# Optimization experiments

Measured on AMD Instinct MI355X. Metric: run time of the kernel, lower is better.

## Reference

```python
import jax, jax.numpy as jnp
import numpy as np

PI = 3.1415927410125732
N = 4096
VELOCITY = 5e-7
RC = 3.15e-6          # collision radius
RR = 8e-6             # repulsion radius
RO = 2.5e-5           # orientation radius (Ra = inf -> inside_Ra all-true)
ALPHA = PI            # field of view; < 2*pi so within_view masking is active
DT_TRANS = 1.4e-14    # translational diffusion DT
DR = 0.0028
GAMMA = 25.0
DT = 0.2              # timestep dt
COLLISION_ITERS = 3   # fixed-iteration version of recursive solve_collisions
EPS = 1e-14


def _c(x):  # [N,2] real -> complex64
    return jax.lax.complex(x[..., 0], x[..., 1])


def _r(z):  # complex -> [..., 2] real
    return jnp.stack([z.real, z.imag], axis=-1)


def _anglediff(a, b):
    # torch get_anglediff: wrap angle(a)-angle(b) into (-pi, pi)
    diff = jnp.angle(a) - jnp.angle(b)
    diff = jnp.where(diff <= -PI, jnp.mod(diff, PI), diff)
    return diff - (diff >= PI) * (2.0 * PI)


def _cossim(a, b):
    # nn.CosineSimilarity(dim=1, eps=1e-14) on view_as_real of complex vectors
    dot = a.real * b.real + a.imag * b.imag
    na = jnp.sqrt(a.real ** 2 + a.imag ** 2 + 1e-30)
    nb = jnp.sqrt(b.real ** 2 + b.imag ** 2 + 1e-30)
    return dot / (jnp.maximum(na, EPS) * jnp.maximum(nb, EPS))


def setup_inputs() -> dict:
    key = jax.random.key(0)
    k1, k2, k3, k4, k5 = jax.random.split(key, 5)
    positions = jax.random.normal(k1, (N, 2), jnp.float32) * 5e-4
    ang = jax.random.uniform(k2, (N,), jnp.float32, -PI, PI)
    orientations = jnp.stack([jnp.cos(ang), jnp.sin(ang)], axis=-1)  # unit complex
    Deltas = jax.random.uniform(k3, (1,), jnp.float32, 0.1, 0.6)
    rot_noise = jax.random.normal(k4, (N,), jnp.float32)
    trans_noise = jax.random.normal(k5, (N, 2), jnp.float32)
    return {"positions": positions, "orientations": orientations, "Deltas": Deltas,
            "rot_noise": rot_noise, "trans_noise": trans_noise}


def reference(positions, orientations, Deltas, rot_noise, trans_noise):
    p = _c(positions)      # [N] complex positions
    u = _c(orientations)   # [N] complex orientations
    n = p.shape[0]
    eye = jnp.eye(n, dtype=bool)

    # pairwise direction/distance: dirs[i,j] = p_j - p_i
    dirs = p[None, :] - p[:, None]
    dists = jnp.abs(dirs)

    inside_Rr = (dists <= RR) & ~eye
    inside_Ro = dists <= RO + RC
    # inside_Ra with Ra = inf is all-True

    # angle between separation vector and orientation of the *neighbor* j
    ang_diff = _anglediff(dirs, u[None, :])
    in_front = ang_diff < PI / 2
    within_view = ang_diff < ALPHA  # alpha < 2*pi branch active

    cdtype = p.dtype
    mask_rr = (inside_Rr & in_front).astype(cdtype)
    mask_ra = within_view.astype(cdtype)  # inside_Ra all True
    mask_ro = (inside_Ro & within_view).astype(cdtype)

    n_r = mask_rr.real.sum(axis=1)
    S = (mask_rr @ p) / jnp.maximum(n_r, 1.0) - p * jnp.sign(n_r)
    d = -S

    n_a = mask_ra.real.sum(axis=1)
    cms = (mask_ra @ p) / jnp.maximum(n_a, 1.0)
    Ps = cms - p * jnp.sign(n_a)

    orientation_sums = mask_ro @ u

    leftturns = Ps * jnp.exp(1j * Deltas)
    rightturns = Ps * jnp.exp(-1j * Deltas)

    # T >= T_release branch: pick the turn most aligned with neighbor orientations
    left_closer = _cossim(leftturns, orientation_sums) >= _cossim(rightturns, orientation_sums)
    best_turns = jnp.where(left_closer, leftturns, rightturns)

    d_abs = jnp.abs(d)
    d_safe = jnp.where(d_abs > 0, d, jnp.ones((), cdtype))
    best_safe = jnp.where(jnp.abs(best_turns) > 0, best_turns, jnp.ones((), cdtype))
    angle_to_target = jnp.where(d_abs > 0, _anglediff(d_safe, u), _anglediff(best_safe, u))

    # rotational_noise = randn * sqrt(2*DR); rotation = exp(i*(dt*Gamma*DR*sin + noise*sqrt(dt)))
    rot = jnp.exp(1j * (DT * GAMMA * DR * jnp.sin(angle_to_target)
                        + rot_noise * np.float32(np.sqrt(2 * DR)) * np.float32(np.sqrt(DT))))

    # complex-normal translational noise (per-component std 1/sqrt(2)) * sqrt(2*DT) * sqrt(dt)
    tn = _c(trans_noise) * np.float32(np.sqrt(0.5)) * np.float32(np.sqrt(2 * DT_TRANS))
    translation = DT * VELOCITY * u + tn * np.float32(np.sqrt(DT))

    def collide(i, pos):
        dd = pos[None, :] - pos[:, None]
        dd_nd = jnp.where(eye, jnp.ones((), pos.dtype), dd)  # avoid 0/0 on diagonal
        ab = jnp.where(eye, 0.0, jnp.abs(dd_nd))
        coll = ab <= 2 * RC - jnp.eye(n, dtype=ab.dtype)
        safe = jnp.where(coll, ab, 1.0)
        move = jnp.where(coll, dd / safe * ((2.1 * RC - ab) * 0.5), jnp.zeros((), pos.dtype))
        return pos - move.sum(axis=1)

    new_p = jax.lax.fori_loop(0, COLLISION_ITERS, collide, p + translation)
    new_u = u * rot

    # pack the 5 complex outputs as real [5, N, 2]
    return jnp.stack([_r(new_p), _r(new_u), _r(orientation_sums), _r(leftturns), _r(rightturns)], axis=0)
```

## Files before the change

### kernel.cpp

```cpp
#include <hip/hip_runtime.h>
#include <math.h>

#define NPART 4096
#define NBLK  512
#define NTHR  256
#define IPB   8
#define SMAX  512

constexpr float RORC   = (float)(2.5e-5 + 3.15e-6);
constexpr float RORC2  = RORC * RORC;
constexpr float RRF    = 8e-6f;
constexpr float RR2    = RRF * RRF;
constexpr float TWORC  = (float)(2.0 * 3.15e-6);
constexpr float TWORC2 = TWORC * TWORC;
constexpr float C21RC  = (float)(2.1 * 3.15e-6);
constexpr float RCAND2 = 1.6e-9f;
constexpr float C_ROT  = (float)(0.2 * 25.0 * 0.0028);
constexpr float C_RN1  = (float)0.07483314773547883;
constexpr float C_SQDT = (float)0.4472135954999579;
constexpr float C_TRV  = (float)(0.2 * 5e-7);
constexpr float C_HALF = (float)0.7071067811865476;
constexpr float C_SQ2T = (float)1.6733200530681511e-07;
constexpr float EPSF   = 1e-14f;

__global__ __launch_bounds__(NTHR) void fused_all(
        const float2* __restrict__ pos, const float2* __restrict__ ori,
        const float* __restrict__ Deltas, const float* __restrict__ rot_noise,
        const float2* __restrict__ trans_noise, float2* __restrict__ out) {
    __shared__ float4   pp4[NPART / 2];
    __shared__ float2   pori_s[NPART];
    __shared__ float    sred[5 * NTHR];
    __shared__ float    res[5][IPB];
    __shared__ unsigned bmap[NPART / 32];
    __shared__ int      Sidx[SMAX];
    __shared__ float2   posS[SMAX];
    __shared__ int      scnt;
    __shared__ int      iloc[IPB];
    float2* ppos_s = (float2*)pp4;

    const int tid  = threadIdx.x;
    if (tid == 0) scnt = 0;
    if (tid < NPART / 32) bmap[tid] = 0u;
    const int il   = tid & (IPB - 1);
    const int seg  = tid / IPB;
    const int gi   = blockIdx.x * IPB + il;
    const int base = seg * 128;

    for (int k = 0; k < NPART / NTHR; ++k) {
        const int j = k * NTHR + tid;
        ppos_s[j] = pos[j];
        pori_s[j] = ori[j];
    }
    __syncthreads();

    const float2 pi = ppos_s[gi];
    float nr = 0.f, sx = 0.f, sy = 0.f, oxs = 0.f, oys = 0.f;
    #pragma unroll 4
    for (int t = 0; t < 64; ++t) {
        const int k2 = (t + seg) & 63;
        const int j0 = base + 2 * k2;
        const float4 v = pp4[j0 >> 1];
        const float dx0 = v.x - pi.x, dy0 = v.y - pi.y;
        const float dx1 = v.z - pi.x, dy1 = v.w - pi.y;
        const float r20 = fmaf(dx0, dx0, dy0 * dy0);
        const float r21 = fmaf(dx1, dx1, dy1 * dy1);
        if (r20 <= RCAND2) {
            const float2 uj = pori_s[j0];
            if (r20 <= RORC2) { oxs += uj.x; oys += uj.y; }
            if (r20 > 0.f) {
                if (r20 <= RR2) {
                    const float dt_ = fmaf(dx0, uj.x, dy0 * uj.y);
                    const float cr_ = fmaf(dy0, uj.x, -dx0 * uj.y);
                    if (!((dt_ <= 0.f) && (cr_ >= 0.f))) { nr += 1.f; sx += v.x; sy += v.y; }
                }
                atomicOr(&bmap[j0 >> 5], 1u << (j0 & 31));
            }
        }
        if (r21 <= RCAND2) {
            const int j1 = j0 + 1;
            const float2 uj = pori_s[j1];
            if (r21 <= RORC2) { oxs += uj.x; oys += uj.y; }
            if (r21 > 0.f) {
                if (r21 <= RR2) {
                    const float dt_ = fmaf(dx1, uj.x, dy1 * uj.y);
                    const float cr_ = fmaf(dy1, uj.x, -dx1 * uj.y);
                    if (!((dt_ <= 0.f) && (cr_ >= 0.f))) { nr += 1.f; sx += v.z; sy += v.w; }
                }
                atomicOr(&bmap[j1 >> 5], 1u << (j1 & 31));
            }
        }
    }
    if (tid < IPB)
        atomicOr(&bmap[gi >> 5], 1u << (gi & 31));
    __syncthreads();
    sred[0 * NTHR + tid] = nr;
    sred[1 * NTHR + tid] = sx;
    sred[2 * NTHR + tid] = sy;
    sred[3 * NTHR + tid] = oxs;
    sred[4 * NTHR + tid] = oys;
    __syncthreads();
    if (tid < 5 * IPB) {
        const int q = tid / IPB, ii = tid & (IPB - 1);
        float acc = 0.f;
        #pragma unroll
        for (int s = 0; s < 32; ++s) acc += sred[q * NTHR + ii + IPB * s];
        res[q][ii] = acc;
    }
    if (tid >= 64 && tid < 64 + NPART / 32) {
        const int w = tid - 64;
        unsigned bits = bmap[w];
        while (bits) {
            const int b = __ffs(bits) - 1;
            bits &= bits - 1;
            const int p = w * 32 + b;
            const int slot = atomicAdd(&scnt, 1);
            if (slot < SMAX) {
                Sidx[slot] = p;
                if ((p >> 3) == (int)blockIdx.x) iloc[p & (IPB - 1)] = slot;
            }
        }
    }
    __syncthreads();
    const int nS = (scnt < SMAX) ? scnt : SMAX;

    float mx = 0.f, my = 0.f;
    for (int k = 0; k < NPART / NTHR; ++k) {
        const float2 v = ppos_s[k * NTHR + tid];
        mx += v.x; my += v.y;
    }
    sred[tid] = mx; sred[NTHR + tid] = my;
    __syncthreads();
    for (int s = NTHR / 2; s > 0; s >>= 1) {
        if (tid < s) { sred[tid] += sred[tid + s]; sred[NTHR + tid] += sred[NTHR + tid + s]; }
        __syncthreads();
    }
    const float cmx = sred[0]    * (1.f / NPART);
    const float cmy = sred[NTHR] * (1.f / NPART);

    for (int m = tid; m < nS; m += NTHR) {
        const int p = Sidx[m];
        const float2 pp = ppos_s[p];
        const float2 uu = pori_s[p];
        const float2 tn = trans_noise[p];
        posS[m] = make_float2(
            pp.x + (C_TRV * uu.x + ((tn.x * C_HALF) * C_SQ2T) * C_SQDT),
            pp.y + (C_TRV * uu.y + ((tn.y * C_HALF) * C_SQ2T) * C_SQDT));
    }

    if (tid < IPB) {
        const int g2 = blockIdx.x * IPB + tid;
        const float2 p = ppos_s[g2];
        const float2 u = pori_s[g2];
        const float nrv = res[0][tid], sxv = res[1][tid], syv = res[2][tid];
        const float osx = res[3][tid], osy = res[4][tid];

        const float inv = 1.f / fmaxf(nrv, 1.f);
        const float sg  = (nrv > 0.f) ? 1.f : 0.f;
        const float Sx = sxv * inv - p.x * sg;
        const float Sy = syv * inv - p.y * sg;
        const float dxv = -Sx, dyv = -Sy;

        const float Psx = cmx - p.x;
        const float Psy = cmy - p.y;

        float sd, cd;
        sincosf(Deltas[0], &sd, &cd);
        const float Lx = Psx * cd - Psy * sd;
        const float Ly = Psx * sd + Psy * cd;
        const float Rx = Psx * cd + Psy * sd;
        const float Ry = Psy * cd - Psx * sd;

        const float no  = fmaxf(sqrtf(osx * osx + osy * osy + 1e-30f), EPSF);
        const float nl  = fmaxf(sqrtf(Lx * Lx + Ly * Ly + 1e-30f), EPSF);
        const float nrr = fmaxf(sqrtf(Rx * Rx + Ry * Ry + 1e-30f), EPSF);
        const float csl = (Lx * osx + Ly * osy) / (nl * no);
        const float csr = (Rx * osx + Ry * osy) / (nrr * no);
        const bool left = (csl >= csr);
        const float bx = left ? Lx : Rx;
        const float by = left ? Ly : Ry;

        float cx, cy;
        if (dxv != 0.f || dyv != 0.f)    { cx = dxv; cy = dyv; }
        else if (bx != 0.f || by != 0.f) { cx = bx;  cy = by;  }
        else                             { cx = 1.f; cy = 0.f; }

        const float dt_ = cx * u.x + cy * u.y;
        const float cr_ = cy * u.x - cx * u.y;
        const float sin_t = cr_ / sqrtf(dt_ * dt_ + cr_ * cr_);

        const float ang = C_ROT * sin_t + (rot_noise[g2] * C_RN1) * C_SQDT;
        float sa, ca;
        sincosf(ang, &sa, &ca);
        const float nux = u.x * ca - u.y * sa;
        const float nuy = u.x * sa + u.y * ca;

        out[1 * NPART + g2] = make_float2(nux, nuy);
        out[2 * NPART + g2] = make_float2(osx, osy);
        out[3 * NPART + g2] = make_float2(Lx, Ly);
        out[4 * NPART + g2] = make_float2(Rx, Ry);
    }
    __syncthreads();

    for (int pass = 0; pass < 3; ++pass) {
        float ax[2] = {0.f, 0.f}, ay[2] = {0.f, 0.f};
        float px[2], py[2];
        #pragma unroll
        for (int q = 0; q < 2; ++q) {
            const int m = tid + q * NTHR;
            if (m < nS) { px[q] = posS[m].x; py[q] = posS[m].y; }
        }
        for (int b = 0; b < nS; ++b) {
            const float2 pb = posS[b];
            #pragma unroll
            for (int q = 0; q < 2; ++q) {
                const int m = tid + q * NTHR;
                if (m < nS) {
                    const float dx = pb.x - px[q], dy = pb.y - py[q];
                    const float r2 = fmaf(dx, dx, dy * dy);
                    if (r2 <= TWORC2 && r2 > 0.f) {
                        const float ab = sqrtf(r2);
                        const float s = (C21RC - ab) * 0.5f / ab;
                        ax[q] = fmaf(dx, s, ax[q]);
                        ay[q] = fmaf(dy, s, ay[q]);
                    }
                }
            }
        }
        __syncthreads();
        #pragma unroll
        for (int q = 0; q < 2; ++q) {
            const int m = tid + q * NTHR;
            if (m < nS) posS[m] = make_float2(px[q] - ax[q], py[q] - ay[q]);
        }
        __syncthreads();
    }
    if (tid < IPB)
        out[0 * NPART + blockIdx.x * IPB + tid] = posS[iloc[tid]];
}

extern "C" void kernel_launch(void* const* d_in, const int* in_sizes, int n_in,
                              void* d_out, int out_size, void* d_ws, size_t ws_size,
                              hipStream_t stream) {
    const float2* pos = (const float2*)d_in[0];
    const float2* ori = (const float2*)d_in[1];
    const float*  del = (const float*)d_in[2];
    const float*  rn  = (const float*)d_in[3];
    const float2* tn  = (const float2*)d_in[4];
    float2* o2 = (float2*)d_out;
    (void)d_ws; (void)ws_size;

    fused_all<<<dim3(NBLK), dim3(NTHR), 0, stream>>>(pos, ori, del, rn, tn, o2);
}
```

Before: 102.0 us.

## Compact candidate neighbor pairs into list, process via atomics; drop orientation smem staging

The all-pairs scan now only tests distances and appends candidate (i,j) pairs to a shared list instead of evaluating the orientation and repulsion logic inline. A second phase walks that compact list, fetches orientations from global memory on demand, and accumulates the per-particle sums with shared atomics. This removes the orientation staging into LDS and the partial-sum reduction across 256 threads. The collision loop is also unrolled four at a time using float4 loads. The risks are atomic contention and silently truncated results if the pair list exceeds its 1024-entry capacity.

```diff
diff --git a/kernel.cpp b/kernel.cpp
--- a/kernel.cpp
+++ b/kernel.cpp
@@ -5,6 +5,7 @@
 #define NBLK  512
 #define NTHR  256
 #define IPB   8
+#define CAPL  1024
 #define SMAX  512
 
 constexpr float RORC   = (float)(2.5e-5 + 3.15e-6);
@@ -28,86 +29,88 @@
         const float* __restrict__ Deltas, const float* __restrict__ rot_noise,
         const float2* __restrict__ trans_noise, float2* __restrict__ out) {
     __shared__ float4   pp4[NPART / 2];
-    __shared__ float2   pori_s[NPART];
-    __shared__ float    sred[5 * NTHR];
+    __shared__ float    sred[2 * NTHR];
     __shared__ float    res[5][IPB];
     __shared__ unsigned bmap[NPART / 32];
+    __shared__ int      lpairs[CAPL];
     __shared__ int      Sidx[SMAX];
-    __shared__ float2   posS[SMAX];
-    __shared__ int      scnt;
+    __shared__ float4   posS4[SMAX / 2];
+    __shared__ int      lcnt, scnt;
     __shared__ int      iloc[IPB];
     float2* ppos_s = (float2*)pp4;
-
-    const int tid  = threadIdx.x;
-    if (tid == 0) scnt = 0;
+    float2* posS   = (float2*)posS4;
+
+    const int tid = threadIdx.x;
+    if (tid == 0) { lcnt = 0; scnt = 0; }
+    if (tid < 5 * IPB) ((float*)res)[tid] = 0.f;
     if (tid < NPART / 32) bmap[tid] = 0u;
-    const int il   = tid & (IPB - 1);
-    const int seg  = tid / IPB;
-    const int gi   = blockIdx.x * IPB + il;
-    const int base = seg * 128;
-
-    for (int k = 0; k < NPART / NTHR; ++k) {
-        const int j = k * NTHR + tid;
-        ppos_s[j] = pos[j];
-        pori_s[j] = ori[j];
-    }
+    const int il  = tid & (IPB - 1);
+    const int seg = tid / IPB;
+    const int gi  = blockIdx.x * IPB + il;
+
+    for (int k = 0; k < NPART / NTHR; ++k)
+        ppos_s[k * NTHR + tid] = pos[k * NTHR + tid];
     __syncthreads();
 
     const float2 pi = ppos_s[gi];
-    float nr = 0.f, sx = 0.f, sy = 0.f, oxs = 0.f, oys = 0.f;
-    #pragma unroll 4
-    for (int t = 0; t < 64; ++t) {
-        const int k2 = (t + seg) & 63;
-        const int j0 = base + 2 * k2;
-        const float4 v = pp4[j0 >> 1];
-        const float dx0 = v.x - pi.x, dy0 = v.y - pi.y;
-        const float dx1 = v.z - pi.x, dy1 = v.w - pi.y;
-        const float r20 = fmaf(dx0, dx0, dy0 * dy0);
-        const float r21 = fmaf(dx1, dx1, dy1 * dy1);
-        if (r20 <= RCAND2) {
-            const float2 uj = pori_s[j0];
-            if (r20 <= RORC2) { oxs += uj.x; oys += uj.y; }
-            if (r20 > 0.f) {
-                if (r20 <= RR2) {
-                    const float dt_ = fmaf(dx0, uj.x, dy0 * uj.y);
-                    const float cr_ = fmaf(dy0, uj.x, -dx0 * uj.y);
-                    if (!((dt_ <= 0.f) && (cr_ >= 0.f))) { nr += 1.f; sx += v.x; sy += v.y; }
-                }
-                atomicOr(&bmap[j0 >> 5], 1u << (j0 & 31));
-            }
-        }
-        if (r21 <= RCAND2) {
-            const int j1 = j0 + 1;
-            const float2 uj = pori_s[j1];
-            if (r21 <= RORC2) { oxs += uj.x; oys += uj.y; }
-            if (r21 > 0.f) {
-                if (r21 <= RR2) {
-                    const float dt_ = fmaf(dx1, uj.x, dy1 * uj.y);
-                    const float cr_ = fmaf(dy1, uj.x, -dx1 * uj.y);
-                    if (!((dt_ <= 0.f) && (cr_ >= 0.f))) { nr += 1.f; sx += v.z; sy += v.w; }
-                }
-                atomicOr(&bmap[j1 >> 5], 1u << (j1 & 31));
-            }
-        }
-    }
-    if (tid < IPB)
-        atomicOr(&bmap[gi >> 5], 1u << (gi & 31));
-    __syncthreads();
-    sred[0 * NTHR + tid] = nr;
-    sred[1 * NTHR + tid] = sx;
-    sred[2 * NTHR + tid] = sy;
-    sred[3 * NTHR + tid] = oxs;
-    sred[4 * NTHR + tid] = oys;
-    __syncthreads();
-    if (tid < 5 * IPB) {
-        const int q = tid / IPB, ii = tid & (IPB - 1);
-        float acc = 0.f;
+    const int base64 = seg * 64;
+    for (int tb = 0; tb < 16; ++tb) {
+        const int kb = (tb + seg) & 15;
+        const float4 v0 = pp4[base64 + kb];
+        const float4 v1 = pp4[base64 + kb + 16];
+        const float4 v2 = pp4[base64 + kb + 32];
+        const float4 v3 = pp4[base64 + kb + 48];
         #pragma unroll
-        for (int s = 0; s < 32; ++s) acc += sred[q * NTHR + ii + IPB * s];
-        res[q][ii] = acc;
-    }
-    if (tid >= 64 && tid < 64 + NPART / 32) {
-        const int w = tid - 64;
+        for (int s = 0; s < 4; ++s) {
+            const float4 v = (s == 0) ? v0 : (s == 1) ? v1 : (s == 2) ? v2 : v3;
+            const int j0 = seg * 128 + 2 * (kb + 16 * s);
+            const float dx0 = v.x - pi.x, dy0 = v.y - pi.y;
+            const float dx1 = v.z - pi.x, dy1 = v.w - pi.y;
+            const float r20 = fmaf(dx0, dx0, dy0 * dy0);
+            const float r21 = fmaf(dx1, dx1, dy1 * dy1);
+            if (fminf(r20, r21) <= RCAND2) {
+                if (r20 <= RCAND2) {
+                    const int slot = atomicAdd(&lcnt, 1);
+                    if (slot < CAPL) lpairs[slot] = (il << 12) | j0;
+                    atomicOr(&bmap[j0 >> 5], 1u << (j0 & 31));
+                }
+                if (r21 <= RCAND2) {
+                    const int j1 = j0 + 1;
+                    const int slot = atomicAdd(&lcnt, 1);
+                    if (slot < CAPL) lpairs[slot] = (il << 12) | j1;
+                    atomicOr(&bmap[j1 >> 5], 1u << (j1 & 31));
+                }
+            }
+        }
+    }
+    __syncthreads();
+
+    const int n_l = (lcnt < CAPL) ? lcnt : CAPL;
+    if (tid < 128) {
+        for (int e = tid; e < n_l; e += 128) {
+            const int code = lpairs[e];
+            const int jil = code >> 12, j = code & (NPART - 1);
+            const float2 pj = ppos_s[j];
+            const float2 pi2 = ppos_s[blockIdx.x * IPB + jil];
+            const float dx = pj.x - pi2.x, dy = pj.y - pi2.y;
+            const float r2 = fmaf(dx, dx, dy * dy);
+            if (r2 <= RORC2) {
+                const float2 uj = ori[j];
+                atomicAdd(&res[3][jil], uj.x);
+                atomicAdd(&res[4][jil], uj.y);
+                if (r2 <= RR2 && r2 > 0.f) {
+                    const float dt_ = fmaf(dx, uj.x, dy * uj.y);
+                    const float cr_ = fmaf(dy, uj.x, -dx * uj.y);
+                    if (!((dt_ <= 0.f) && (cr_ >= 0.f))) {
+                        atomicAdd(&res[0][jil], 1.f);
+                        atomicAdd(&res[1][jil], pj.x);
+                        atomicAdd(&res[2][jil], pj.y);
+                    }
+                }
+            }
+        }
+    } else {
+        const int w = tid - 128;
         unsigned bits = bmap[w];
         while (bits) {
             const int b = __ffs(bits) - 1;
@@ -123,6 +126,16 @@
     __syncthreads();
     const int nS = (scnt < SMAX) ? scnt : SMAX;
 
+    for (int m = tid; m < nS; m += NTHR) {
+        const int p = Sidx[m];
+        const float2 pp = ppos_s[p];
+        const float2 uu = ori[p];
+        const float2 tn = trans_noise[p];
+        posS[m] = make_float2(
+            pp.x + (C_TRV * uu.x + ((tn.x * C_HALF) * C_SQ2T) * C_SQDT),
+            pp.y + (C_TRV * uu.y + ((tn.y * C_HALF) * C_SQ2T) * C_SQDT));
+    }
+
     float mx = 0.f, my = 0.f;
     for (int k = 0; k < NPART / NTHR; ++k) {
         const float2 v = ppos_s[k * NTHR + tid];
@@ -137,20 +150,10 @@
     const float cmx = sred[0]    * (1.f / NPART);
     const float cmy = sred[NTHR] * (1.f / NPART);
 
-    for (int m = tid; m < nS; m += NTHR) {
-        const int p = Sidx[m];
-        const float2 pp = ppos_s[p];
-        const float2 uu = pori_s[p];
-        const float2 tn = trans_noise[p];
-        posS[m] = make_float2(
-            pp.x + (C_TRV * uu.x + ((tn.x * C_HALF) * C_SQ2T) * C_SQDT),
-            pp.y + (C_TRV * uu.y + ((tn.y * C_HALF) * C_SQ2T) * C_SQDT));
-    }
-
     if (tid < IPB) {
         const int g2 = blockIdx.x * IPB + tid;
         const float2 p = ppos_s[g2];
-        const float2 u = pori_s[g2];
+        const float2 u = ori[g2];
         const float nrv = res[0][tid], sxv = res[1][tid], syv = res[2][tid];
         const float osx = res[3][tid], osy = res[4][tid];
 
@@ -191,10 +194,8 @@
         const float ang = C_ROT * sin_t + (rot_noise[g2] * C_RN1) * C_SQDT;
         float sa, ca;
         sincosf(ang, &sa, &ca);
-        const float nux = u.x * ca - u.y * sa;
-        const float nuy = u.x * sa + u.y * ca;
-
-        out[1 * NPART + g2] = make_float2(nux, nuy);
+        out[1 * NPART + g2] = make_float2(u.x * ca - u.y * sa,
+                                          u.x * sa + u.y * ca);
         out[2 * NPART + g2] = make_float2(osx, osy);
         out[3 * NPART + g2] = make_float2(Lx, Ly);
         out[4 * NPART + g2] = make_float2(Rx, Ry);
@@ -202,26 +203,49 @@
     __syncthreads();
 
     for (int pass = 0; pass < 3; ++pass) {
-        float ax[2] = {0.f, 0.f}, ay[2] = {0.f, 0.f};
-        float px[2], py[2];
+        float px[2], py[2], ax[2] = {0.f, 0.f}, ay[2] = {0.f, 0.f};
+        bool  mv[2];
         #pragma unroll
         for (int q = 0; q < 2; ++q) {
             const int m = tid + q * NTHR;
-            if (m < nS) { px[q] = posS[m].x; py[q] = posS[m].y; }
-        }
-        for (int b = 0; b < nS; ++b) {
+            mv[q] = (m < nS);
+            if (mv[q]) { px[q] = posS[m].x; py[q] = posS[m].y; }
+        }
+        int b = 0;
+        for (; b + 4 <= nS; b += 4) {
+            const float4 w0 = posS4[(b >> 1)];
+            const float4 w1 = posS4[(b >> 1) + 1];
+            const float bxs[4] = {w0.x, w0.z, w1.x, w1.z};
+            const float bys[4] = {w0.y, w0.w, w1.y, w1.w};
+            #pragma unroll
+            for (int s = 0; s < 4; ++s) {
+                #pragma unroll
+                for (int q = 0; q < 2; ++q) {
+                    if (mv[q]) {
+                        const float dx = bxs[s] - px[q], dy = bys[s] - py[q];
+                        const float r2 = fmaf(dx, dx, dy * dy);
+                        if (r2 <= TWORC2 && r2 > 0.f) {
+                            const float ab = sqrtf(r2);
+                            const float sc = (C21RC - ab) * 0.5f / ab;
+                            ax[q] = fmaf(dx, sc, ax[q]);
+                            ay[q] = fmaf(dy, sc, ay[q]);
+                        }
+                    }
+                }
+            }
+        }
+        for (; b < nS; ++b) {
             const float2 pb = posS[b];
             #pragma unroll
             for (int q = 0; q < 2; ++q) {
-                const int m = tid + q * NTHR;
-                if (m < nS) {
+                if (mv[q]) {
                     const float dx = pb.x - px[q], dy = pb.y - py[q];
                     const float r2 = fmaf(dx, dx, dy * dy);
                     if (r2 <= TWORC2 && r2 > 0.f) {
                         const float ab = sqrtf(r2);
-                        const float s = (C21RC - ab) * 0.5f / ab;
-                        ax[q] = fmaf(dx, s, ax[q]);
-                        ay[q] = fmaf(dy, s, ay[q]);
+                        const float sc = (C21RC - ab) * 0.5f / ab;
+                        ax[q] = fmaf(dx, sc, ax[q]);
+                        ay[q] = fmaf(dy, sc, ay[q]);
                     }
                 }
             }
```

Measured after the change: 96.23 us. -5.6%, faster.
